# Kernel optimization log

Hardware: AMD Instinct MI355X
Metric: run time of the kernel (lower is better)

## Reference

```python
import jax, jax.numpy as jnp
import numpy as np

H_DIM = 1024
N_HEADS = 16
MAX_T = 2048
NUM_INPUTS = 3   # period of (return, state, action) tokens
RET_ORDER = 2


def _build_mask(T):
    # causal lower-triangular mask with mgdt selective column masking
    mask = jnp.tril(jnp.ones((T, T), dtype=bool))
    # columns period+ret_order-1, period+ret_order-1+period, ... are zeroed
    cols = np.arange(NUM_INPUTS + RET_ORDER - 1, MAX_T, NUM_INPUTS)
    cols = cols[cols < T]
    mask = mask.at[:, cols].set(False)
    return mask  # [T, T] bool


def setup_inputs() -> dict:
    key = jax.random.key(0)
    ks = jax.random.split(key, 9)
    B, T, C = 2, 2048, H_DIM
    s = 1.0 / np.sqrt(C)
    return {
        "x": jax.random.normal(ks[0], (B, T, C), dtype=jnp.float32),
        "Wq": jax.random.normal(ks[1], (C, C), dtype=jnp.float32) * s,
        "bq": jnp.zeros((C,), dtype=jnp.float32),
        "Wk": jax.random.normal(ks[2], (C, C), dtype=jnp.float32) * s,
        "bk": jnp.zeros((C,), dtype=jnp.float32),
        "Wv": jax.random.normal(ks[3], (C, C), dtype=jnp.float32) * s,
        "bv": jnp.zeros((C,), dtype=jnp.float32),
        "Wp": jax.random.normal(ks[4], (C, C), dtype=jnp.float32) * s,
        "bp": jnp.zeros((C,), dtype=jnp.float32),
    }


def reference(x, Wq, bq, Wk, bk, Wv, bv, Wp, bp):
    B, T, C = x.shape
    N = N_HEADS
    D = C // N
    # QKV projections; weights stored (in, out) so x @ W
    q = (x @ Wq + bq).reshape(B, T, N, D).transpose(0, 2, 1, 3)  # [B,N,T,D]
    k = (x @ Wk + bk).reshape(B, T, N, D).transpose(0, 2, 1, 3)
    v = (x @ Wv + bv).reshape(B, T, N, D).transpose(0, 2, 1, 3)

    scale = 1.0 / np.sqrt(D).astype(np.float32)
    scores = jnp.einsum("bntd,bnsd->bnts", q, k) * scale  # [B,N,T,T]
    mask = _build_mask(T)  # [T,T]
    scores = jnp.where(mask[None, None], scores, -jnp.inf)
    attn = jax.nn.softmax(scores, axis=-1)
    out = jnp.einsum("bnts,bnsd->bntd", attn, v)  # [B,N,T,D]
    out = out.transpose(0, 2, 1, 3).reshape(B, T, C)
    return out @ Wp + bp
```

## Files before the change

### kernel.cpp

```cpp
#include <hip/hip_runtime.h>

#define AS_GLOBAL __attribute__((address_space(1)))
#define AS_LDS    __attribute__((address_space(3)))

typedef __bf16 bf16;
typedef __bf16 bf16x4 __attribute__((ext_vector_type(4)));
typedef __bf16 bf16x8 __attribute__((ext_vector_type(8)));
typedef float  f32x4  __attribute__((ext_vector_type(4)));
typedef unsigned short u16x8 __attribute__((ext_vector_type(8)));

__device__ __forceinline__ void gload16(const void* g, void* l) {
  __builtin_amdgcn_global_load_lds((const AS_GLOBAL unsigned int*)g,
                                   (AS_LDS unsigned int*)l, 16, 0, 0);
}

__device__ __forceinline__ void* swz(void* base, int row, int bytecol) {
  return (char*)base + row * 128 + (bytecol ^ ((row & 7) << 4));
}

__device__ __forceinline__ int keptcnt(int X) { return X - ((X - 2) < 0 ? 0 : (X - 2) / 3); }
__device__ __forceinline__ int ci2s(int ci) {
  return 3 * ((ci - 2) >> 1) + 2 + ((ci - 2) & 1);
}
__device__ __forceinline__ int ci2s_full(int ci) {
  return ci < 2 ? ci : ci2s(ci);
}

__global__ __launch_bounds__(256) void k_prep(const float* __restrict__ x,
                                              const float* __restrict__ Wq,
                                              const float* __restrict__ Wk,
                                              const float* __restrict__ Wv,
                                              const float* __restrict__ Wp,
                                              const float* __restrict__ bq,
                                              const float* __restrict__ bk,
                                              const float* __restrict__ bv,
                                              bf16* __restrict__ xb,
                                              bf16* __restrict__ wqkvT,
                                              bf16* __restrict__ wpT,
                                              float* __restrict__ bc) {
  int blk = blockIdx.x;
  if (blk < 2048) {
    int i = blk * 256 + threadIdx.x;
    const float4* p = (const float4*)(x + (size_t)i * 8);
    float4 a = p[0], b = p[1];
    bf16x8 v;
    v[0] = (bf16)a.x; v[1] = (bf16)a.y; v[2] = (bf16)a.z; v[3] = (bf16)a.w;
    v[4] = (bf16)b.x; v[5] = (bf16)b.y; v[6] = (bf16)b.z; v[7] = (bf16)b.w;
    *(bf16x8*)(xb + (size_t)i * 8) = v;
  } else if (blk < 4096) {
    int wblk = blk - 2048;
    int sel = wblk >> 9;
    const float* W = (sel == 0) ? Wq : (sel == 1) ? Wk : (sel == 2) ? Wv : Wp;
    bf16* dst = (sel < 3) ? (wqkvT + (size_t)sel * 1024 * 1024) : wpT;
    int lin = (wblk & 511) * 256 + threadIdx.x;
    int n = lin & 1023, kc = lin >> 10;
    bf16x8 v;
#pragma unroll
    for (int j = 0; j < 8; ++j) v[j] = (bf16)W[(size_t)(kc * 8 + j) * 1024 + n];
    *(bf16x8*)&dst[(size_t)n * 1024 + kc * 8] = v;
  } else {
    int i = (blk - 4096) * 256 + threadIdx.x;
    bc[i] = (i < 1024) ? bq[i] : (i < 2048 ? bk[i - 1024] : bv[i - 2048]);
  }
}

__global__ __launch_bounds__(256) void k_compact(const bf16* __restrict__ qkv,
                                                 bf16* __restrict__ kc,
                                                 bf16* __restrict__ vc) {
  __shared__ unsigned L[32 * 65];
  int blk = blockIdx.x;
  int tid = threadIdx.x;
  if (blk < 1408) {
    int bh = blk / 44, rc = blk % 44;
    int b = bh >> 4, h = bh & 15;
    int rr = tid >> 3, ch = tid & 7;
    int ci = rc * 32 + rr;
    int s = ci2s_full(ci);
    bf16x8 v = {};
    if (s < 2048)
      v = *(const bf16x8*)&qkv[(size_t)(b * 2048 + s) * 3072 + 1024 + h * 64 + ch * 8];
    *(bf16x8*)&kc[((size_t)bh * 1408 + ci) * 64 + ch * 8] = v;
  } else {
    int vblk = blk - 1408;
    int bh = vblk / 22, cc = vblk % 22;
    int b = bh >> 4, h = bh & 15;
    int ci0 = cc * 64;
    int p = tid >> 3, d0 = (tid & 7) * 8;
    int s0 = ci2s_full(ci0 + 2 * p), s1 = ci2s_full(ci0 + 2 * p + 1);
    u16x8 e = {}, od = {};
    if (s0 < 2048)
      e = *(const u16x8*)&qkv[(size_t)(b * 2048 + s0) * 3072 + 2048 + h * 64 + d0];
    if (s1 < 2048)
      od = *(const u16x8*)&qkv[(size_t)(b * 2048 + s1) * 3072 + 2048 + h * 64 + d0];
#pragma unroll
    for (int k2 = 0; k2 < 8; ++k2)
      L[p * 65 + d0 + k2] = (unsigned)e[k2] | ((unsigned)od[k2] << 16);
    __syncthreads();
#pragma unroll
    for (int it = 0; it < 2; ++it) {
      int d = it * 32 + (tid >> 3), jg = tid & 7;
      unsigned q4[4];
#pragma unroll
      for (int jj = 0; jj < 4; ++jj) q4[jj] = L[(jg * 4 + jj) * 65 + d];
      *(uint4*)&vc[((size_t)bh * 64 + d) * 1408 + ci0 + jg * 8] = *(uint4*)q4;
    }
  }
}

template <typename OutT>
__global__ __launch_bounds__(256) void k_gemm_bt(const bf16* __restrict__ A,
                                                 const bf16* __restrict__ Bt,
                                                 const float* __restrict__ bias,
                                                 OutT* __restrict__ C,
                                                 int K, int N) {
  __shared__ bf16 As[2][128 * 32];
  __shared__ bf16 Bs[2][128 * 32];
  const int tid = threadIdx.x;
  const int w = tid >> 6, l = tid & 63, g = l >> 4, c = l & 15;
  const int wr = w >> 1, wc = w & 1;
  int lin = blockIdx.y * gridDim.x + blockIdx.x;
  int chunk = (gridDim.x * gridDim.y) >> 3;
  int nl = (lin & 7) * chunk + (lin >> 3);
  const int row0 = (nl % gridDim.x) * 128, col0 = (nl / gridDim.x) * 128;
  f32x4 acc[4][4] = {};

  auto stage = [&](int buf, int k0) {
#pragma unroll
    for (int it = 0; it < 2; ++it) {
      int idx = it * 256 + tid;
      int r = idx >> 2, cc = idx & 3;
      int jj = cc ^ ((r >> 1) & 3);
      gload16(A  + (size_t)(row0 + r) * K + k0 + jj * 8, &As[buf][idx * 8]);
      gload16(Bt + (size_t)(col0 + r) * K + k0 + jj * 8, &Bs[buf][idx * 8]);
    }
  };

  stage(0, 0);
  int cur = 0;
#pragma unroll 1
  for (int k0 = 0; k0 < K; k0 += 32) {
    __syncthreads();

    if (k0 + 32 < K) stage(cur ^ 1, k0 + 32);

    bf16x8 af[4], bfr[4];
#pragma unroll
    for (int m = 0; m < 4; ++m) {
      int row = wr * 64 + m * 16 + c;
      af[m] = *(const bf16x8*)&As[cur][row * 32 + (g ^ ((row >> 1) & 3)) * 8];
    }
#pragma unroll
    for (int n = 0; n < 4; ++n) {
      int row = wc * 64 + n * 16 + c;
      bfr[n] = *(const bf16x8*)&Bs[cur][row * 32 + (g ^ ((row >> 1) & 3)) * 8];
    }
#pragma unroll
    for (int m = 0; m < 4; ++m)
#pragma unroll
      for (int n = 0; n < 4; ++n)
        acc[m][n] = __builtin_amdgcn_mfma_f32_16x16x32_bf16(af[m], bfr[n],
                                                            acc[m][n], 0, 0, 0);
    cur ^= 1;
  }

#pragma unroll
  for (int m = 0; m < 4; ++m) {
    int row = row0 + wr * 64 + m * 16 + g * 4;
#pragma unroll
    for (int n = 0; n < 4; ++n) {
      int col = col0 + wc * 64 + n * 16 + c;
      float bv = bias[col];
#pragma unroll
      for (int r = 0; r < 4; ++r) {
        float v = acc[m][n][r] + bv;
        C[(size_t)(row + r) * N + col] = (OutT)v;
      }
    }
  }
}

__global__ __launch_bounds__(256, 4) void k_attn(const bf16* __restrict__ qkv,
                                                 const bf16* __restrict__ kc,
                                                 const bf16* __restrict__ vc,
                                                 bf16* __restrict__ att) {
  const int idx = blockIdx.x;
  const int slot = idx >> 8, j = idx & 255;
  const int r8 = j >> 5, bh = j & 31;
  const int b = bh >> 4, h = bh & 15;
  int qt;
  switch (slot) {
    case 0: qt = r8;       break;
    case 1: qt = 31 - r8;  break;
    case 2: qt = r8 + 8;   break;
    default: qt = 23 - r8; break;
  }

  const int tid = threadIdx.x;
  const int w = tid >> 6, l = tid & 63, g = l >> 4, c = l & 15;
  const int qw0 = qt * 64 + w * 16;
  const int qq = qw0 + c;

  const int nt = (keptcnt(qt * 64 + 64) + 63) >> 6;
  const int tmaskw = keptcnt(qw0 + 1) >> 6;

  __shared__ bf16 Ks[2][64 * 64];
  __shared__ bf16 Vs[2][64 * 64];
  __shared__ bf16 Plds[4][16 * 64];

  const bf16* kgc = kc + (size_t)bh * 1408 * 64;
  const bf16* vgc = vc + (size_t)bh * 64 * 1408;

  auto stage = [&](int buf, int t) {
    int s0 = t * 64;
#pragma unroll
    for (int it = 0; it < 2; ++it) {
      int ch = it * 256 + tid;
      int rr = ch >> 3, jj = (ch & 7) ^ (rr & 7);
      gload16(kgc + (size_t)(s0 + rr) * 64 + jj * 8, &Ks[buf][ch * 8]);
      gload16(vgc + (size_t)rr * 1408 + s0 + jj * 8, &Vs[buf][ch * 8]);
    }
  };

  const bf16* qb = qkv + (size_t)(b * 2048 + qq) * 3072 + h * 64 + g * 8;
  bf16x8 qf0 = *(const bf16x8*)qb;
  bf16x8 qf1 = *(const bf16x8*)(qb + 32);
#pragma unroll
  for (int jq = 0; jq < 8; ++jq) {
    qf0[jq] = (bf16)((float)qf0[jq] * 0.125f);
    qf1[jq] = (bf16)((float)qf1[jq] * 0.125f);
  }

  f32x4 o[4] = {};
  float mrow = -1e30f, ell = 0.f;

  stage(0, 0);

  int cur = 0;
#pragma unroll 1
  for (int t = 0; t < nt; ++t) {
    __syncthreads();

    if (t + 1 < nt) stage(cur ^ 1, t + 1);

    f32x4 ss[4] = {};
#pragma unroll
    for (int st = 0; st < 4; ++st) {
      bf16x8 ka  = *(const bf16x8*)swz(&Ks[cur][0], st * 16 + c, g * 16);
      bf16x8 kb2 = *(const bf16x8*)swz(&Ks[cur][0], st * 16 + c, 64 + g * 16);
      ss[st] = __builtin_amdgcn_mfma_f32_16x16x32_bf16(ka,  qf0, ss[st], 0, 0, 0);
      ss[st] = __builtin_amdgcn_mfma_f32_16x16x32_bf16(kb2, qf1, ss[st], 0, 0, 0);
    }

    float mloc = -1e30f;
    if (t >= tmaskw) {
#pragma unroll
      for (int st = 0; st < 4; ++st)
#pragma unroll
        for (int r = 0; r < 4; ++r) {
          int ci = t * 64 + st * 16 + g * 4 + r;
          int s = ci2s(ci);
          if (t == 0) s = (ci < 2) ? ci : s;
          float v = (s <= qq) ? ss[st][r] : -1e30f;
          ss[st][r] = v;
          mloc = fmaxf(mloc, v);
        }
    } else {
#pragma unroll
      for (int st = 0; st < 4; ++st)
#pragma unroll
        for (int r = 0; r < 4; ++r) mloc = fmaxf(mloc, ss[st][r]);
    }
    mloc = fmaxf(mloc, __shfl_xor(mloc, 16));
    mloc = fmaxf(mloc, __shfl_xor(mloc, 32));

    float mn = fmaxf(mrow, mloc);
    float al = __expf(mrow - mn);
    mrow = mn;
    float rsum = 0.f;
#pragma unroll
    for (int st = 0; st < 4; ++st) {
      float p0 = __expf(ss[st][0] - mn);
      float p1 = __expf(ss[st][1] - mn);
      float p2 = __expf(ss[st][2] - mn);
      float p3 = __expf(ss[st][3] - mn);
      rsum += (p0 + p1) + (p2 + p3);
      bf16x4 pk = {(bf16)p0, (bf16)p1, (bf16)p2, (bf16)p3};
      *(bf16x4*)swz(&Plds[w][0], c, st * 32 + g * 8) = pk;
    }
    rsum += __shfl_xor(rsum, 16);
    rsum += __shfl_xor(rsum, 32);
    ell = ell * al + rsum;
#pragma unroll
    for (int dc = 0; dc < 4; ++dc)
#pragma unroll
      for (int r = 0; r < 4; ++r) o[dc][r] *= al;

    asm volatile("s_waitcnt lgkmcnt(0)" ::: "memory");
    __builtin_amdgcn_sched_barrier(0);

#pragma unroll
    for (int kk = 0; kk < 2; ++kk) {
      bf16x8 pf = *(const bf16x8*)swz(&Plds[w][0], c, kk * 64 + g * 16);
#pragma unroll
      for (int dc = 0; dc < 4; ++dc) {
        bf16x8 vf = *(const bf16x8*)swz(&Vs[cur][0], dc * 16 + c, kk * 64 + g * 16);
        o[dc] = __builtin_amdgcn_mfma_f32_16x16x32_bf16(vf, pf, o[dc], 0, 0, 0);
      }
    }

    cur ^= 1;
  }

  float inv = 1.f / ell;
#pragma unroll
  for (int dc = 0; dc < 4; ++dc) {
    bf16x4 ok4 = {(bf16)(o[dc][0] * inv), (bf16)(o[dc][1] * inv),
                  (bf16)(o[dc][2] * inv), (bf16)(o[dc][3] * inv)};
    *(bf16x4*)swz(&Plds[w][0], c, dc * 32 + g * 8) = ok4;
  }
  asm volatile("s_waitcnt lgkmcnt(0)" ::: "memory");
  __builtin_amdgcn_sched_barrier(0);
#pragma unroll
  for (int p = 0; p < 2; ++p) {
    int row = p * 8 + (l >> 3);
    bf16x8 vrow = *(const bf16x8*)swz(&Plds[w][0], row, (l & 7) * 16);
    *(bf16x8*)&att[(size_t)(b * 2048 + qt * 64 + w * 16 + row) * 1024 +
                   h * 64 + (l & 7) * 8] = vrow;
  }
}

extern "C" void kernel_launch(void* const* d_in, const int* in_sizes, int n_in,
                              void* d_out, int out_size, void* d_ws, size_t ws_size,
                              hipStream_t stream) {
  const float* x  = (const float*)d_in[0];
  const float* Wq = (const float*)d_in[1];
  const float* bq = (const float*)d_in[2];
  const float* Wk = (const float*)d_in[3];
  const float* bk = (const float*)d_in[4];
  const float* Wv = (const float*)d_in[5];
  const float* bv = (const float*)d_in[6];
  const float* Wp = (const float*)d_in[7];
  const float* bp = (const float*)d_in[8];
  float* out = (float*)d_out;

  char* ws = (char*)d_ws;
  const size_t MB = 1024 * 1024;
  bf16*  xb    = (bf16*)(ws);
  bf16*  wqkvT = (bf16*)(ws + 8 * MB);
  bf16*  wpT   = (bf16*)(ws + 14 * MB);
  float* bcat  = (float*)(ws + 16 * MB);
  bf16*  qkv   = (bf16*)(ws + 17 * MB);
  bf16*  vcb   = (bf16*)(ws + 41 * MB);
  bf16*  kcb   = (bf16*)(ws + 47 * MB);
  bf16*  att   = xb;

  k_prep<<<4108, 256, 0, stream>>>(x, Wq, Wk, Wv, Wp, bq, bk, bv,
                                   xb, wqkvT, wpT, bcat);
  k_gemm_bt<bf16><<<dim3(32, 24), 256, 0, stream>>>(xb, wqkvT, bcat, qkv, 1024, 3072);
  k_compact<<<2112, 256, 0, stream>>>(qkv, kcb, vcb);
  k_attn<<<1024, 256, 0, stream>>>(qkv, kcb, vcb, att);
  k_gemm_bt<float><<<dim3(32, 8), 256, 0, stream>>>(att, wpT, bp, out, 1024, 1024);
}
```

Before: 107.1 us.

## Process two query tiles per attention block and gather K directly from qkv

Each attention block now handles two 64-row query tiles (A and B) that share every staged K/V tile, which halves the grid and the K/V loads per query row. K is no longer copied into a compacted buffer; the staging loop gathers K rows from qkv through the kept-column index map, so the compact kernel only transposes V. The cost is doubled accumulator and score registers, launch bounds lowered to 2 blocks per CU, fewer blocks for load balancing, and less contiguous K loads.

```diff
diff --git a/kernel.cpp b/kernel.cpp
--- a/kernel.cpp
+++ b/kernel.cpp
@@ -65,45 +65,31 @@
 }
 
 __global__ __launch_bounds__(256) void k_compact(const bf16* __restrict__ qkv,
-                                                 bf16* __restrict__ kc,
                                                  bf16* __restrict__ vc) {
   __shared__ unsigned L[32 * 65];
   int blk = blockIdx.x;
   int tid = threadIdx.x;
-  if (blk < 1408) {
-    int bh = blk / 44, rc = blk % 44;
-    int b = bh >> 4, h = bh & 15;
-    int rr = tid >> 3, ch = tid & 7;
-    int ci = rc * 32 + rr;
-    int s = ci2s_full(ci);
-    bf16x8 v = {};
-    if (s < 2048)
-      v = *(const bf16x8*)&qkv[(size_t)(b * 2048 + s) * 3072 + 1024 + h * 64 + ch * 8];
-    *(bf16x8*)&kc[((size_t)bh * 1408 + ci) * 64 + ch * 8] = v;
-  } else {
-    int vblk = blk - 1408;
-    int bh = vblk / 22, cc = vblk % 22;
-    int b = bh >> 4, h = bh & 15;
-    int ci0 = cc * 64;
-    int p = tid >> 3, d0 = (tid & 7) * 8;
-    int s0 = ci2s_full(ci0 + 2 * p), s1 = ci2s_full(ci0 + 2 * p + 1);
-    u16x8 e = {}, od = {};
-    if (s0 < 2048)
-      e = *(const u16x8*)&qkv[(size_t)(b * 2048 + s0) * 3072 + 2048 + h * 64 + d0];
-    if (s1 < 2048)
-      od = *(const u16x8*)&qkv[(size_t)(b * 2048 + s1) * 3072 + 2048 + h * 64 + d0];
-#pragma unroll
-    for (int k2 = 0; k2 < 8; ++k2)
-      L[p * 65 + d0 + k2] = (unsigned)e[k2] | ((unsigned)od[k2] << 16);
-    __syncthreads();
-#pragma unroll
-    for (int it = 0; it < 2; ++it) {
-      int d = it * 32 + (tid >> 3), jg = tid & 7;
-      unsigned q4[4];
-#pragma unroll
-      for (int jj = 0; jj < 4; ++jj) q4[jj] = L[(jg * 4 + jj) * 65 + d];
-      *(uint4*)&vc[((size_t)bh * 64 + d) * 1408 + ci0 + jg * 8] = *(uint4*)q4;
-    }
+  int bh = blk / 22, cc = blk % 22;
+  int b = bh >> 4, h = bh & 15;
+  int ci0 = cc * 64;
+  int p = tid >> 3, d0 = (tid & 7) * 8;
+  int s0 = ci2s_full(ci0 + 2 * p), s1 = ci2s_full(ci0 + 2 * p + 1);
+  u16x8 e = {}, od = {};
+  if (s0 < 2048)
+    e = *(const u16x8*)&qkv[(size_t)(b * 2048 + s0) * 3072 + 2048 + h * 64 + d0];
+  if (s1 < 2048)
+    od = *(const u16x8*)&qkv[(size_t)(b * 2048 + s1) * 3072 + 2048 + h * 64 + d0];
+#pragma unroll
+  for (int k2 = 0; k2 < 8; ++k2)
+    L[p * 65 + d0 + k2] = (unsigned)e[k2] | ((unsigned)od[k2] << 16);
+  __syncthreads();
+#pragma unroll
+  for (int it = 0; it < 2; ++it) {
+    int d = it * 32 + (tid >> 3), jg = tid & 7;
+    unsigned q4[4];
+#pragma unroll
+    for (int jj = 0; jj < 4; ++jj) q4[jj] = L[(jg * 4 + jj) * 65 + d];
+    *(uint4*)&vc[((size_t)bh * 64 + d) * 1408 + ci0 + jg * 8] = *(uint4*)q4;
   }
 }
 
@@ -179,35 +165,28 @@
   }
 }
 
-__global__ __launch_bounds__(256, 4) void k_attn(const bf16* __restrict__ qkv,
-                                                 const bf16* __restrict__ kc,
+__global__ __launch_bounds__(256, 2) void k_attn(const bf16* __restrict__ qkv,
                                                  const bf16* __restrict__ vc,
                                                  bf16* __restrict__ att) {
   const int idx = blockIdx.x;
   const int slot = idx >> 8, j = idx & 255;
   const int r8 = j >> 5, bh = j & 31;
   const int b = bh >> 4, h = bh & 15;
-  int qt;
-  switch (slot) {
-    case 0: qt = r8;       break;
-    case 1: qt = 31 - r8;  break;
-    case 2: qt = r8 + 8;   break;
-    default: qt = 23 - r8; break;
-  }
+  const int qt2 = (slot == 0) ? r8 : 15 - r8;
 
   const int tid = threadIdx.x;
   const int w = tid >> 6, l = tid & 63, g = l >> 4, c = l & 15;
-  const int qw0 = qt * 64 + w * 16;
-  const int qq = qw0 + c;
-
-  const int nt = (keptcnt(qt * 64 + 64) + 63) >> 6;
-  const int tmaskw = keptcnt(qw0 + 1) >> 6;
+  const int qA = qt2 * 128 + w * 16, qB = qA + 64;
+  const int qqA = qA + c, qqB = qB + c;
+
+  const int nt = (keptcnt(qt2 * 128 + 128) + 63) >> 6;
+  const int tmA = keptcnt(qA + 1) >> 6;
+  const int tmB = keptcnt(qB + 1) >> 6;
 
   __shared__ bf16 Ks[2][64 * 64];
   __shared__ bf16 Vs[2][64 * 64];
-  __shared__ bf16 Plds[4][16 * 64];
-
-  const bf16* kgc = kc + (size_t)bh * 1408 * 64;
+  __shared__ bf16 Plds[4][2][16 * 64];
+
   const bf16* vgc = vc + (size_t)bh * 64 * 1408;
 
   auto stage = [&](int buf, int t) {
@@ -216,22 +195,28 @@
     for (int it = 0; it < 2; ++it) {
       int ch = it * 256 + tid;
       int rr = ch >> 3, jj = (ch & 7) ^ (rr & 7);
-      gload16(kgc + (size_t)(s0 + rr) * 64 + jj * 8, &Ks[buf][ch * 8]);
+      int s = ci2s_full(s0 + rr);
+      s = (s < 2048) ? s : 0;
+      gload16(qkv + (size_t)(b * 2048 + s) * 3072 + 1024 + h * 64 + jj * 8,
+              &Ks[buf][ch * 8]);
       gload16(vgc + (size_t)rr * 1408 + s0 + jj * 8, &Vs[buf][ch * 8]);
     }
   };
 
-  const bf16* qb = qkv + (size_t)(b * 2048 + qq) * 3072 + h * 64 + g * 8;
-  bf16x8 qf0 = *(const bf16x8*)qb;
-  bf16x8 qf1 = *(const bf16x8*)(qb + 32);
+  const bf16* qbA = qkv + (size_t)(b * 2048 + qqA) * 3072 + h * 64 + g * 8;
+  const bf16* qbB = qkv + (size_t)(b * 2048 + qqB) * 3072 + h * 64 + g * 8;
+  bf16x8 qf0A = *(const bf16x8*)qbA, qf1A = *(const bf16x8*)(qbA + 32);
+  bf16x8 qf0B = *(const bf16x8*)qbB, qf1B = *(const bf16x8*)(qbB + 32);
 #pragma unroll
   for (int jq = 0; jq < 8; ++jq) {
-    qf0[jq] = (bf16)((float)qf0[jq] * 0.125f);
-    qf1[jq] = (bf16)((float)qf1[jq] * 0.125f);
-  }
-
-  f32x4 o[4] = {};
-  float mrow = -1e30f, ell = 0.f;
+    qf0A[jq] = (bf16)((float)qf0A[jq] * 0.125f);
+    qf1A[jq] = (bf16)((float)qf1A[jq] * 0.125f);
+    qf0B[jq] = (bf16)((float)qf0B[jq] * 0.125f);
+    qf1B[jq] = (bf16)((float)qf1B[jq] * 0.125f);
+  }
+
+  f32x4 oA[4] = {}, oB[4] = {};
+  float mA = -1e30f, lA = 0.f, mB = -1e30f, lB = 0.f;
 
   stage(0, 0);
 
@@ -242,90 +227,143 @@
 
     if (t + 1 < nt) stage(cur ^ 1, t + 1);
 
-    f32x4 ss[4] = {};
+    f32x4 sA[4] = {}, sB[4] = {};
 #pragma unroll
     for (int st = 0; st < 4; ++st) {
       bf16x8 ka  = *(const bf16x8*)swz(&Ks[cur][0], st * 16 + c, g * 16);
       bf16x8 kb2 = *(const bf16x8*)swz(&Ks[cur][0], st * 16 + c, 64 + g * 16);
-      ss[st] = __builtin_amdgcn_mfma_f32_16x16x32_bf16(ka,  qf0, ss[st], 0, 0, 0);
-      ss[st] = __builtin_amdgcn_mfma_f32_16x16x32_bf16(kb2, qf1, ss[st], 0, 0, 0);
-    }
-
-    float mloc = -1e30f;
-    if (t >= tmaskw) {
-#pragma unroll
-      for (int st = 0; st < 4; ++st)
-#pragma unroll
-        for (int r = 0; r < 4; ++r) {
-          int ci = t * 64 + st * 16 + g * 4 + r;
-          int s = ci2s(ci);
-          if (t == 0) s = (ci < 2) ? ci : s;
-          float v = (s <= qq) ? ss[st][r] : -1e30f;
-          ss[st][r] = v;
-          mloc = fmaxf(mloc, v);
-        }
-    } else {
-#pragma unroll
-      for (int st = 0; st < 4; ++st)
-#pragma unroll
-        for (int r = 0; r < 4; ++r) mloc = fmaxf(mloc, ss[st][r]);
-    }
-    mloc = fmaxf(mloc, __shfl_xor(mloc, 16));
-    mloc = fmaxf(mloc, __shfl_xor(mloc, 32));
-
-    float mn = fmaxf(mrow, mloc);
-    float al = __expf(mrow - mn);
-    mrow = mn;
-    float rsum = 0.f;
-#pragma unroll
-    for (int st = 0; st < 4; ++st) {
-      float p0 = __expf(ss[st][0] - mn);
-      float p1 = __expf(ss[st][1] - mn);
-      float p2 = __expf(ss[st][2] - mn);
-      float p3 = __expf(ss[st][3] - mn);
-      rsum += (p0 + p1) + (p2 + p3);
-      bf16x4 pk = {(bf16)p0, (bf16)p1, (bf16)p2, (bf16)p3};
-      *(bf16x4*)swz(&Plds[w][0], c, st * 32 + g * 8) = pk;
-    }
-    rsum += __shfl_xor(rsum, 16);
-    rsum += __shfl_xor(rsum, 32);
-    ell = ell * al + rsum;
-#pragma unroll
-    for (int dc = 0; dc < 4; ++dc)
-#pragma unroll
-      for (int r = 0; r < 4; ++r) o[dc][r] *= al;
+      sA[st] = __builtin_amdgcn_mfma_f32_16x16x32_bf16(ka,  qf0A, sA[st], 0, 0, 0);
+      sA[st] = __builtin_amdgcn_mfma_f32_16x16x32_bf16(kb2, qf1A, sA[st], 0, 0, 0);
+      sB[st] = __builtin_amdgcn_mfma_f32_16x16x32_bf16(ka,  qf0B, sB[st], 0, 0, 0);
+      sB[st] = __builtin_amdgcn_mfma_f32_16x16x32_bf16(kb2, qf1B, sB[st], 0, 0, 0);
+    }
+
+    {
+      float mloc = -1e30f;
+      if (t >= tmA) {
+#pragma unroll
+        for (int st = 0; st < 4; ++st)
+#pragma unroll
+          for (int r = 0; r < 4; ++r) {
+            int ci = t * 64 + st * 16 + g * 4 + r;
+            int s = ci2s(ci);
+            if (t == 0) s = (ci < 2) ? ci : s;
+            float v = (s <= qqA) ? sA[st][r] : -1e30f;
+            sA[st][r] = v;
+            mloc = fmaxf(mloc, v);
+          }
+      } else {
+#pragma unroll
+        for (int st = 0; st < 4; ++st)
+#pragma unroll
+          for (int r = 0; r < 4; ++r) mloc = fmaxf(mloc, sA[st][r]);
+      }
+      mloc = fmaxf(mloc, __shfl_xor(mloc, 16));
+      mloc = fmaxf(mloc, __shfl_xor(mloc, 32));
+      float mn = fmaxf(mA, mloc);
+      float al = __expf(mA - mn);
+      mA = mn;
+      float rs = 0.f;
+#pragma unroll
+      for (int st = 0; st < 4; ++st) {
+        float p0 = __expf(sA[st][0] - mn);
+        float p1 = __expf(sA[st][1] - mn);
+        float p2 = __expf(sA[st][2] - mn);
+        float p3 = __expf(sA[st][3] - mn);
+        rs += (p0 + p1) + (p2 + p3);
+        bf16x4 pk = {(bf16)p0, (bf16)p1, (bf16)p2, (bf16)p3};
+        *(bf16x4*)swz(&Plds[w][0][0], c, st * 32 + g * 8) = pk;
+      }
+      rs += __shfl_xor(rs, 16);
+      rs += __shfl_xor(rs, 32);
+      lA = lA * al + rs;
+#pragma unroll
+      for (int dc = 0; dc < 4; ++dc)
+#pragma unroll
+        for (int r = 0; r < 4; ++r) oA[dc][r] *= al;
+    }
+    {
+      float mloc = -1e30f;
+      if (t >= tmB) {
+#pragma unroll
+        for (int st = 0; st < 4; ++st)
+#pragma unroll
+          for (int r = 0; r < 4; ++r) {
+            int ci = t * 64 + st * 16 + g * 4 + r;
+            int s = ci2s(ci);
+            if (t == 0) s = (ci < 2) ? ci : s;
+            float v = (s <= qqB) ? sB[st][r] : -1e30f;
+            sB[st][r] = v;
+            mloc = fmaxf(mloc, v);
+          }
+      } else {
+#pragma unroll
+        for (int st = 0; st < 4; ++st)
+#pragma unroll
+          for (int r = 0; r < 4; ++r) mloc = fmaxf(mloc, sB[st][r]);
+      }
+      mloc = fmaxf(mloc, __shfl_xor(mloc, 16));
+      mloc = fmaxf(mloc, __shfl_xor(mloc, 32));
+      float mn = fmaxf(mB, mloc);
+      float al = __expf(mB - mn);
+      mB = mn;
+      float rs = 0.f;
+#pragma unroll
+      for (int st = 0; st < 4; ++st) {
+        float p0 = __expf(sB[st][0] - mn);
+        float p1 = __expf(sB[st][1] - mn);
+        float p2 = __expf(sB[st][2] - mn);
+        float p3 = __expf(sB[st][3] - mn);
+        rs += (p0 + p1) + (p2 + p3);
+        bf16x4 pk = {(bf16)p0, (bf16)p1, (bf16)p2, (bf16)p3};
+        *(bf16x4*)swz(&Plds[w][1][0], c, st * 32 + g * 8) = pk;
+      }
+      rs += __shfl_xor(rs, 16);
+      rs += __shfl_xor(rs, 32);
+      lB = lB * al + rs;
+#pragma unroll
+      for (int dc = 0; dc < 4; ++dc)
+#pragma unroll
+        for (int r = 0; r < 4; ++r) oB[dc][r] *= al;
+    }
 
     asm volatile("s_waitcnt lgkmcnt(0)" ::: "memory");
     __builtin_amdgcn_sched_barrier(0);
 
 #pragma unroll
     for (int kk = 0; kk < 2; ++kk) {
-      bf16x8 pf = *(const bf16x8*)swz(&Plds[w][0], c, kk * 64 + g * 16);
+      bf16x8 pfA = *(const bf16x8*)swz(&Plds[w][0][0], c, kk * 64 + g * 16);
+      bf16x8 pfB = *(const bf16x8*)swz(&Plds[w][1][0], c, kk * 64 + g * 16);
 #pragma unroll
       for (int dc = 0; dc < 4; ++dc) {
         bf16x8 vf = *(const bf16x8*)swz(&Vs[cur][0], dc * 16 + c, kk * 64 + g * 16);
-        o[dc] = __builtin_amdgcn_mfma_f32_16x16x32_bf16(vf, pf, o[dc], 0, 0, 0);
+        oA[dc] = __builtin_amdgcn_mfma_f32_16x16x32_bf16(vf, pfA, oA[dc], 0, 0, 0);
+        oB[dc] = __builtin_amdgcn_mfma_f32_16x16x32_bf16(vf, pfB, oB[dc], 0, 0, 0);
       }
     }
 
     cur ^= 1;
   }
 
-  float inv = 1.f / ell;
+  float invA = 1.f / lA, invB = 1.f / lB;
 #pragma unroll
   for (int dc = 0; dc < 4; ++dc) {
-    bf16x4 ok4 = {(bf16)(o[dc][0] * inv), (bf16)(o[dc][1] * inv),
-                  (bf16)(o[dc][2] * inv), (bf16)(o[dc][3] * inv)};
-    *(bf16x4*)swz(&Plds[w][0], c, dc * 32 + g * 8) = ok4;
+    bf16x4 a4 = {(bf16)(oA[dc][0] * invA), (bf16)(oA[dc][1] * invA),
+                 (bf16)(oA[dc][2] * invA), (bf16)(oA[dc][3] * invA)};
+    bf16x4 b4 = {(bf16)(oB[dc][0] * invB), (bf16)(oB[dc][1] * invB),
+                 (bf16)(oB[dc][2] * invB), (bf16)(oB[dc][3] * invB)};
+    *(bf16x4*)swz(&Plds[w][0][0], c, dc * 32 + g * 8) = a4;
+    *(bf16x4*)swz(&Plds[w][1][0], c, dc * 32 + g * 8) = b4;
   }
   asm volatile("s_waitcnt lgkmcnt(0)" ::: "memory");
   __builtin_amdgcn_sched_barrier(0);
 #pragma unroll
   for (int p = 0; p < 2; ++p) {
     int row = p * 8 + (l >> 3);
-    bf16x8 vrow = *(const bf16x8*)swz(&Plds[w][0], row, (l & 7) * 16);
-    *(bf16x8*)&att[(size_t)(b * 2048 + qt * 64 + w * 16 + row) * 1024 +
-                   h * 64 + (l & 7) * 8] = vrow;
+    bf16x8 va = *(const bf16x8*)swz(&Plds[w][0][0], row, (l & 7) * 16);
+    bf16x8 vb = *(const bf16x8*)swz(&Plds[w][1][0], row, (l & 7) * 16);
+    *(bf16x8*)&att[(size_t)(b * 2048 + qA + row) * 1024 + h * 64 + (l & 7) * 8] = va;
+    *(bf16x8*)&att[(size_t)(b * 2048 + qB + row) * 1024 + h * 64 + (l & 7) * 8] = vb;
   }
 }
 
@@ -351,13 +389,12 @@
   float* bcat  = (float*)(ws + 16 * MB);
   bf16*  qkv   = (bf16*)(ws + 17 * MB);
   bf16*  vcb   = (bf16*)(ws + 41 * MB);
-  bf16*  kcb   = (bf16*)(ws + 47 * MB);
   bf16*  att   = xb;
 
   k_prep<<<4108, 256, 0, stream>>>(x, Wq, Wk, Wv, Wp, bq, bk, bv,
                                    xb, wqkvT, wpT, bcat);
   k_gemm_bt<bf16><<<dim3(32, 24), 256, 0, stream>>>(xb, wqkvT, bcat, qkv, 1024, 3072);
-  k_compact<<<2112, 256, 0, stream>>>(qkv, kcb, vcb);
-  k_attn<<<1024, 256, 0, stream>>>(qkv, kcb, vcb, att);
+  k_compact<<<704, 256, 0, stream>>>(qkv, vcb);
+  k_attn<<<512, 256, 0, stream>>>(qkv, vcb, att);
   k_gemm_bt<float><<<dim3(32, 8), 256, 0, stream>>>(att, wpT, bp, out, 1024, 1024);
 }
```

Measured after the change: 115.6 us. +8.0%, slower.
